# Kernel tuning notes

Measured on AMD Instinct MI355X. Metric: run time of the kernel, lower is better.

The kernel has to match this reference:

```python
import jax, jax.numpy as jnp
import numpy as np

HDIM = 1024
CDIM = 256
TEMPER = 10.0
IGNORE_OUT = 0.0
EPS = 1e-6


def setup_inputs() -> dict:
    key = jax.random.key(0)
    ks = jax.random.split(key, 6)
    B, T, D = 2, 128, 384
    x = jax.random.normal(ks[0], (B, T, D), jnp.float32)
    y = jax.random.normal(ks[1], (B, T, D), jnp.float32)
    # xavier-normal style init for the two linear layers
    W_enc = jax.random.normal(ks[2], (D, HDIM), jnp.float32) * np.sqrt(2.0 / (D + HDIM))
    b_enc = jnp.zeros((HDIM,), jnp.float32)
    W_dec = jax.random.normal(ks[3], (HDIM, D), jnp.float32) * np.sqrt(2.0 / (D + HDIM))
    b_dec = jnp.zeros((D,), jnp.float32)
    return {"x": x, "y": y, "W_enc": W_enc, "b_enc": b_enc, "W_dec": W_dec, "b_dec": b_dec}


def reference(x, y, W_enc, b_enc, W_dec, b_dec):
    B, T, D = x.shape
    n_iter = HDIM // CDIM
    pad = D - 1
    # shift_idx[s, j] = s + j : window of width D at offset s, s in [0, 2D-2]
    shift_idx = jnp.arange(2 * D - 1)[:, None] + jnp.arange(D)[None, :]

    seq_mask = (y == IGNORE_OUT)                       # (B,T,D) bool
    denom_seq = jnp.sum(~seq_mask).astype(x.dtype)
    qn = jnp.linalg.norm(y, axis=-1)                   # (B,T)

    mask_prev = None
    x_dis, losses = [], []
    for _ in range(n_iter):
        # --- _pad_for_shift: (B,T,2D-1,D) shifted windows of x ---
        kp = jnp.pad(x, ((0, 0), (0, 0), (pad, pad)))  # (B,T,3D-2)
        kpt = kp[..., shift_idx]                       # (B,T,2D-1,D)
        # --- _score (cos) + argmax over shifts ---
        kn = jnp.linalg.norm(kpt, axis=-1)             # (B,T,2D-1)
        sim = jnp.einsum('btsd,btd->bts', kpt, y) / (qn[..., None] * kn + EPS)
        sim = jnp.where(jnp.isnan(sim), 0.0, sim)
        theta = jnp.argmax(sim, axis=-1)               # (B,T) int
        x_opt = jnp.take_along_axis(kpt, theta[..., None, None], axis=-2)[..., 0, :]  # (B,T,D)
        # --- attention: elementwise cos-scaled score, temp softmax, detached ---
        dn = (jnp.linalg.norm(x_opt, axis=-1, keepdims=True)
              * jnp.linalg.norm(y, axis=-1, keepdims=True) + EPS)
        attn = jax.nn.softmax((x_opt * y / dn) / TEMPER, axis=-1)
        attn = jnp.where(jnp.isnan(attn), 0.0, attn)
        attn = jax.lax.stop_gradient(attn)
        x_attn = x_opt * attn
        # --- _reverse_pad_for_shift: window at offset 2D-2-theta ---
        kp2 = jnp.pad(x_attn, ((0, 0), (0, 0), (pad, pad)))
        rev_idx = (2 * D - 2 - theta)[..., None] + jnp.arange(D)  # (B,T,D)
        x_ele = jnp.take_along_axis(kp2, rev_idx, axis=-1)         # (B,T,D)
        # --- self_net: encoder -> top-k sparsify -> decoder_self ---
        h = x_ele @ W_enc + b_enc                      # (B,T,HDIM)
        if mask_prev is not None:
            h = jnp.where(mask_prev > 0, 1e-10, h)
        _, idx_top = jax.lax.top_k(h, CDIM)            # (B,T,CDIM)
        flat = idx_top.reshape(B * T, CDIM)
        mask_cur = jnp.zeros((B * T, HDIM), x.dtype).at[
            jnp.arange(B * T)[:, None], flat].set(1.0).reshape(B, T, HDIM)
        if mask_prev is None:
            mask_prev = mask_cur
        else:
            mask_prev = mask_prev + mask_cur - mask_prev * mask_cur
        h = h * mask_cur
        out = h @ W_dec + b_dec                        # (B,T,D)
        x_dis.append(out)
        # --- SeqLoss (masked MSE, mean-reduced by count of valid elems) ---
        err = jnp.where(seq_mask, 0.0, (out - x) ** 2) / denom_seq
        losses.append(jnp.sum(err))
    return jnp.stack(x_dis), jnp.stack(losses)
```

## Files before the change

kernel.cpp:

```cpp
#include <hip/hip_runtime.h>
#include <hip/hip_fp16.h>
#include <math.h>

#define DD 384
#define HD 1024
#define CD 256
#define NS 765
#define NITER 4
#define NROWS 256
#define TEMPER_F 10.0f
#define EPSF 1e-6f
#define CUTF 1e-10f

typedef unsigned long long u64;
typedef unsigned int u32;
typedef _Float16 hh2 __attribute__((ext_vector_type(2)));

__device__ __forceinline__ u32 flipf(float f) {
    u32 u = __float_as_uint(f);
    return u ^ ((u32)((int)u >> 31) | 0x80000000u);
}
__device__ __forceinline__ u32 packh2(float a, float b) {
    __half2 p = __floats2half2_rn(a, b);
    return __builtin_bit_cast(u32, p);
}
__device__ __forceinline__ float dot2(u32 a, u32 b, float c) {
#if __has_builtin(__builtin_amdgcn_fdot2)
    return __builtin_amdgcn_fdot2(__builtin_bit_cast(hh2, a),
                                  __builtin_bit_cast(hh2, b), c, false);
#else
    __half2 ah = __builtin_bit_cast(__half2, a);
    __half2 bh = __builtin_bit_cast(__half2, b);
    return fmaf(__half2float(ah.y), __half2float(bh.y),
           fmaf(__half2float(ah.x), __half2float(bh.x), c));
#endif
}

__global__ __launch_bounds__(256) void convert_kernel(
    const float* __restrict__ We, const float* __restrict__ Wd,
    uint4* __restrict__ wencp4, uint2* __restrict__ wd16)
{
    const int t = blockIdx.x * 256 + threadIdx.x;
    if (t < 192 * 256) {
        const int j2 = t >> 8, c4 = t & 255;
        float4 a = *(const float4*)&We[(2 * j2)     * HD + 4 * c4];
        float4 b = *(const float4*)&We[(2 * j2 + 1) * HD + 4 * c4];
        wencp4[j2 * 256 + c4] = make_uint4(packh2(a.x, b.x), packh2(a.y, b.y),
                                           packh2(a.z, b.z), packh2(a.w, b.w));
    }
    for (int i = t; i < (HD * DD) / 4; i += 65536) {
        float4 v = ((const float4*)Wd)[i];
        wd16[i] = make_uint2(packh2(v.x, v.y), packh2(v.z, v.w));
    }
}

__global__ __launch_bounds__(1024) void fused_kernel(
    const float* __restrict__ x, const float* __restrict__ y,
    const u32* __restrict__ wencp, const float* __restrict__ benc,
    const u32* __restrict__ wdec16, const float* __restrict__ bdec,
    float* __restrict__ out_xdis, float* __restrict__ lossp,
    int* __restrict__ ycnt)
{
    const int row  = blockIdx.x;
    const int tid  = threadIdx.x;
    const int lane = tid & 63;
    const int wid  = tid >> 6;

    __shared__ __align__(16) float xpad[1152];
    __shared__ __align__(16) float yr[DD];
    __shared__ float xa[DD];
    __shared__ __align__(16) float xe_s[DD];
    __shared__ u32   xep[192];
    __shared__ __align__(16) float part[4][HD];
    __shared__ __align__(16) uint2 dec2[HD];
    __shared__ __align__(16) float4 dpart[8][96];
    __shared__ float wred[16];
    __shared__ int   wredi[16];
    __shared__ float wredn[16];
    __shared__ int   wbase16[16];
    __shared__ float s_sc[4];
    __shared__ int   s_theta;
    __shared__ u32   s_b[3];
    __shared__ int   sbinB[3], srankB[3], s_cc[3];
    __shared__ u32   cand[3][64];
    __shared__ int   wcls[128];
    __shared__ int   sbase[128];
    __shared__ int   cnt8[8];
    __shared__ float loss4[NITER];

    const float* xrow = x + row * DD;
    const float* yrow = y + row * DD;

    for (int i = tid; i < 1152; i += 1024)
        xpad[i] = (i >= DD - 1 && i < 2 * DD - 1) ? xrow[i - (DD - 1)] : 0.f;
    if (tid < DD) yr[tid] = yrow[tid];
    __syncthreads();

    if (tid < DD) {
        float p = yr[tid] * yr[tid];
        int   c = (yr[tid] != 0.f) ? 1 : 0;
        for (int o = 32; o; o >>= 1) {
            p += __shfl_xor(p, o, 64);
            c += __shfl_xor(c, o, 64);
        }
        if (lane == 0) { wred[wid] = p; wredi[wid] = c; }
    }
    __syncthreads();
    if (tid == 0) {
        float s = 0.f; int c = 0;
        for (int w = 0; w < 6; ++w) { s += wred[w]; c += wredi[w]; }
        s_sc[0] = sqrtf(s);
        ycnt[row] = c;
    }
    __syncthreads();
    const float qn = s_sc[0];

    float bv = -INFINITY; int bs = 0x7fffffff; float bn = 0.f;
    if (tid < 192) {
        const float4* xp4 = (const float4*)xpad;
        const float4* yp4 = (const float4*)yr;
        float4 A = xp4[tid];
        const float f0 = A.x * A.x, f1 = A.y * A.y, f2 = A.z * A.z;
        float d0 = 0.f, d1 = 0.f, d2 = 0.f, d3 = 0.f, n0 = 0.f;
#pragma unroll 4
        for (int jc = 0; jc < 96; ++jc) {
            float4 B = xp4[tid + jc + 1];
            float4 Y = yp4[jc];
            d0 += A.x * Y.x; d0 += A.y * Y.y; d0 += A.z * Y.z; d0 += A.w * Y.w;
            d1 += A.y * Y.x; d1 += A.z * Y.y; d1 += A.w * Y.z; d1 += B.x * Y.w;
            d2 += A.z * Y.x; d2 += A.w * Y.y; d2 += B.x * Y.z; d2 += B.y * Y.w;
            d3 += A.w * Y.x; d3 += B.x * Y.y; d3 += B.y * Y.z; d3 += B.z * Y.w;
            n0 += A.x * A.x; n0 += A.y * A.y; n0 += A.z * A.z; n0 += A.w * A.w;
            A = B;
        }
        const float n1 = n0 - f0 + A.x * A.x;
        const float n2 = n1 - f1 + A.y * A.y;
        const float n3 = n2 - f2 + A.z * A.z;
        const int s0 = 4 * tid;
        float sim0 = d0 / (qn * sqrtf(n0) + EPSF);
        float sim1 = d1 / (qn * sqrtf(n1) + EPSF);
        float sim2 = d2 / (qn * sqrtf(n2) + EPSF);
        float sim3 = d3 / (qn * sqrtf(n3) + EPSF);
        bv = sim0; bs = s0; bn = n0;
        if (s0 + 1 < NS && sim1 > bv) { bv = sim1; bs = s0 + 1; bn = n1; }
        if (s0 + 2 < NS && sim2 > bv) { bv = sim2; bs = s0 + 2; bn = n2; }
        if (s0 + 3 < NS && sim3 > bv) { bv = sim3; bs = s0 + 3; bn = n3; }
    }
    for (int o = 32; o; o >>= 1) {
        float v2 = __shfl_xor(bv, o, 64);
        int   i2 = __shfl_xor(bs, o, 64);
        float n2 = __shfl_xor(bn, o, 64);
        if (v2 > bv || (v2 == bv && i2 < bs)) { bv = v2; bs = i2; bn = n2; }
    }
    if (lane == 0) { wred[wid] = bv; wredi[wid] = bs; wredn[wid] = bn; }
    __syncthreads();
    if (tid == 0) {
        float v = wred[0]; int b = wredi[0]; float nn = wredn[0];
        for (int w = 1; w < 16; ++w)
            if (wred[w] > v || (wred[w] == v && wredi[w] < b)) {
                v = wred[w]; b = wredi[w]; nn = wredn[w];
            }
        s_theta = b;
        s_sc[1] = sqrtf(nn) * qn + EPSF;
    }
    __syncthreads();
    const int theta = s_theta;
    const float dn = s_sc[1];

    float xo = 0.f, ez = 0.f;
    if (tid < DD) {
        xo = xpad[theta + tid];
        ez = expf((xo * yr[tid] / dn) / TEMPER_F);
        float p = ez;
        for (int o = 32; o; o >>= 1) p += __shfl_xor(p, o, 64);
        if (lane == 0) wred[wid] = p;
    }
    __syncthreads();
    if (tid == 0) {
        float s = 0.f;
        for (int w = 0; w < 6; ++w) s += wred[w];
        s_sc[3] = s;
    }
    __syncthreads();
    if (tid < DD) xa[tid] = xo * (ez / s_sc[3]);
    __syncthreads();
    if (tid < DD) {
        int sj = tid - (theta - (DD - 1));
        xe_s[tid] = (sj >= 0 && sj < DD) ? xa[sj] : 0.f;
    }
    __syncthreads();
    if (tid < 192) xep[tid] = packh2(xe_s[2 * tid], xe_s[2 * tid + 1]);
    __syncthreads();

    {
        const int ks = tid >> 8;
        const int c4 = tid & 255;
        const uint4* wq = (const uint4*)wencp + (size_t)(ks * 48) * 256 + c4;
        const u32* xb = xep + ks * 48;
        float4 acc = make_float4(0.f, 0.f, 0.f, 0.f);
#pragma unroll 8
        for (int j2 = 0; j2 < 48; ++j2) {
            u32 xv = xb[j2];
            uint4 w = wq[(size_t)j2 * 256];
            acc.x = dot2(xv, w.x, acc.x);
            acc.y = dot2(xv, w.y, acc.y);
            acc.z = dot2(xv, w.z, acc.z);
            acc.w = dot2(xv, w.w, acc.w);
        }
        *(float4*)&part[ks][4 * c4] = acc;
    }
    if (tid < 8) cnt8[tid] = 0;
    if (tid < NITER) loss4[tid] = 0.f;
    __syncthreads();

    const float oh = part[0][tid] + part[1][tid] + part[2][tid] + part[3][tid]
                   + benc[tid];
    const u32 okey = ~flipf(oh);
    __syncthreads();

    u32* hist = (u32*)part;
    {
        hist[tid] = 0; hist[tid + 1024] = 0;
        hist[tid + 2048] = 0; hist[tid + 3072] = 0;
        if (tid < 192) cand[tid >> 6][tid & 63] = 0xFFFFFFFFu;
        if (tid < 3) s_cc[tid] = 0;
        __syncthreads();
        atomicAdd(&hist[okey >> 20], 1u);
        __syncthreads();
        const int t4 = tid << 2;
        const u32 l0 = hist[t4], l1 = hist[t4 + 1], l2 = hist[t4 + 2], l3 = hist[t4 + 3];
        const int s = (int)(l0 + l1 + l2 + l3);
        int inc = s;
        for (int o = 1; o < 64; o <<= 1) {
            int u = __shfl_up(inc, o, 64);
            if (lane >= o) inc += u;
        }
        if (lane == 63) wredi[wid] = inc;
        __syncthreads();
        if (tid == 0) {
            int acc = 0;
            for (int w = 0; w < 16; ++w) { wbase16[w] = acc; acc += wredi[w]; }
        }
        __syncthreads();
        const int c0 = wbase16[wid] + inc - s;
        const int c1 = c0 + (int)l0, c2 = c1 + (int)l1, c3 = c2 + (int)l2;
        const int c4e = c3 + (int)l3;
#pragma unroll
        for (int i = 0; i < 3; ++i) {
            const int R = 255 + (i << 8);
            if (R >= c0 && R < c1)      { sbinB[i] = t4;     srankB[i] = R - c0; }
            else if (R >= c1 && R < c2) { sbinB[i] = t4 + 1; srankB[i] = R - c1; }
            else if (R >= c2 && R < c3) { sbinB[i] = t4 + 2; srankB[i] = R - c2; }
            else if (R >= c3 && R < c4e){ sbinB[i] = t4 + 3; srankB[i] = R - c3; }
        }
        __syncthreads();
        const int myb = (int)(okey >> 20);
#pragma unroll
        for (int i = 0; i < 3; ++i) {
            if (myb == sbinB[i]) {
                int slot = atomicAdd(&s_cc[i], 1);
                if (slot < 64) cand[i][slot] = okey;
            }
        }
        __syncthreads();
        if (wid < 3) {
            u32 v = cand[wid][lane];
            for (int k2 = 2; k2 <= 64; k2 <<= 1) {
                for (int j = k2 >> 1; j > 0; j >>= 1) {
                    u32 p = __shfl_xor(v, j, 64);
                    const bool takeMin = ((lane & j) == 0) == ((lane & k2) == 0);
                    v = takeMin ? (v < p ? v : p) : (v > p ? v : p);
                }
            }
            if (lane == srankB[wid]) s_b[wid] = v;
        }
        __syncthreads();
    }
    const u32 b1 = s_b[0], b2 = s_b[1], b3 = s_b[2];

    {
        const int myk = (okey <= b1) ? 0 : (okey <= b2) ? 1 : (okey <= b3) ? 2 : 3;
        const int cls = 2 * myk + ((oh > CUTF) ? 0 : 1);
        int myprefix = 0;
        const u64 ltmask = (1ull << lane) - 1;
#pragma unroll
        for (int c = 0; c < 8; ++c) {
            u64 m = __ballot(cls == c);
            if (cls == c) myprefix = __popcll(m & ltmask);
            if (lane == 0) {
                wcls[c * 16 + wid] = (int)__popcll(m);
                atomicAdd(&cnt8[c], (int)__popcll(m));
            }
        }
        __syncthreads();
        if (tid < 128) {
            int v = wcls[tid];
            int inc = v;
            for (int o = 1; o < 64; o <<= 1) {
                int t2 = __shfl_up(inc, o, 64);
                if (lane >= o) inc += t2;
            }
            sbase[tid] = inc - v;
        }
        __syncthreads();
        if (tid >= 64 && tid < 128) sbase[tid] += sbase[63] + wcls[63];
        __syncthreads();
        const int slot = sbase[cls * 16 + wid] + myprefix;
        dec2[slot] = make_uint2(__float_as_uint(oh), (u32)tid * 192u);
    }
    __syncthreads();

    {
        const int g8 = tid >> 7;
        const int k  = g8 >> 1;
        const int hf = g8 & 1;
        const int gg = tid & 127;
        const bool active = (gg < 96);
        int n = 0;
        if (active) n = (k == 0) ? CD : cnt8[2 * k];
        int r  = hf * 128;
        int r1 = n < r + 128 ? n : r + 128;
        if (r1 < r) r1 = r;
        float4 acc = make_float4(0.f, 0.f, 0.f, 0.f);
        const u32* wd = wdec16 + 2 * gg;
        const int base = k * CD;
        for (; r + 8 <= r1; r += 8) {
#pragma unroll
            for (int q = 0; q < 8; q += 2) {
                uint4 dv = *(const uint4*)&dec2[base + r + q];
                u32 vp = packh2(__uint_as_float(dv.x), __uint_as_float(dv.z));
                uint2 w0 = *(const uint2*)(wd + dv.y);
                uint2 w1 = *(const uint2*)(wd + dv.w);
                u32 p0 = (w0.x & 0xffffu) | (w1.x << 16);
                u32 p1 = (w0.x >> 16) | (w1.x & 0xffff0000u);
                u32 p2 = (w0.y & 0xffffu) | (w1.y << 16);
                u32 p3 = (w0.y >> 16) | (w1.y & 0xffff0000u);
                acc.x = dot2(vp, p0, acc.x);
                acc.y = dot2(vp, p1, acc.y);
                acc.z = dot2(vp, p2, acc.z);
                acc.w = dot2(vp, p3, acc.w);
            }
        }
        for (; r + 2 <= r1; r += 2) {
            uint4 dv = *(const uint4*)&dec2[base + r];
            u32 vp = packh2(__uint_as_float(dv.x), __uint_as_float(dv.z));
            uint2 w0 = *(const uint2*)(wd + dv.y);
            uint2 w1 = *(const uint2*)(wd + dv.w);
            u32 p0 = (w0.x & 0xffffu) | (w1.x << 16);
            u32 p1 = (w0.x >> 16) | (w1.x & 0xffff0000u);
            u32 p2 = (w0.y & 0xffffu) | (w1.y << 16);
            u32 p3 = (w0.y >> 16) | (w1.y & 0xffff0000u);
            acc.x = dot2(vp, p0, acc.x);
            acc.y = dot2(vp, p1, acc.y);
            acc.z = dot2(vp, p2, acc.z);
            acc.w = dot2(vp, p3, acc.w);
        }
        if (r < r1) {
            uint2 dv = dec2[base + r];
            float v0 = __uint_as_float(dv.x);
            uint2 w0 = *(const uint2*)(wd + dv.y);
            u32 vlo = packh2(v0, 0.f), vhi = packh2(0.f, v0);
            acc.x = dot2(vlo, w0.x, acc.x);
            acc.y = dot2(vhi, w0.x, acc.y);
            acc.z = dot2(vlo, w0.y, acc.z);
            acc.w = dot2(vhi, w0.y, acc.w);
        }
        if (active) dpart[g8][gg] = acc;
    }
    __syncthreads();

    {
        float l = 0.f;
        if (tid < 512) {
            const int k2 = tid >> 7;
            const int q  = tid & 127;
            if (q < 96) {
                float4 a = dpart[2 * k2][q];
                float4 b = dpart[2 * k2 + 1][q];
                float4 bb = *(const float4*)&bdec[4 * q];
                float4 o4;
                o4.x = a.x + b.x + bb.x;
                o4.y = a.y + b.y + bb.y;
                o4.z = a.z + b.z + bb.z;
                o4.w = a.w + b.w + bb.w;
                *(float4*)&out_xdis[((size_t)k2 * NROWS + row) * DD + 4 * q] = o4;
                float4 xv = *(const float4*)&xrow[4 * q];
                float4 yv = *(const float4*)&yr[4 * q];
                float ee;
                ee = o4.x - xv.x; if (yv.x != 0.f) l += ee * ee;
                ee = o4.y - xv.y; if (yv.y != 0.f) l += ee * ee;
                ee = o4.z - xv.z; if (yv.z != 0.f) l += ee * ee;
                ee = o4.w - xv.w; if (yv.w != 0.f) l += ee * ee;
            }
        }
        for (int o = 32; o; o >>= 1) l += __shfl_xor(l, o, 64);
        if (tid < 512 && lane == 0) atomicAdd(&loss4[tid >> 7], l);
    }
    __syncthreads();
    if (tid < NITER) lossp[row * NITER + tid] = loss4[tid];
}

__global__ __launch_bounds__(256) void finalize2(
    const float* __restrict__ lossp, const int* __restrict__ ycnt,
    float* __restrict__ losses)
{
    const int tid = threadIdx.x, lane = tid & 63, w = tid >> 6;
    __shared__ int ctot[4];
    int c = ycnt[tid];
    for (int o = 32; o; o >>= 1) c += __shfl_xor(c, o, 64);
    if (lane == 0) ctot[w] = c;
    __syncthreads();
    const int total = ctot[0] + ctot[1] + ctot[2] + ctot[3];
    float s = lossp[lane * NITER + w] + lossp[(lane + 64) * NITER + w]
            + lossp[(lane + 128) * NITER + w] + lossp[(lane + 192) * NITER + w];
    for (int o = 32; o; o >>= 1) s += __shfl_xor(s, o, 64);
    if (lane == 0) losses[w] = s / (float)total;
}

extern "C" void kernel_launch(void* const* d_in, const int* in_sizes, int n_in,
                              void* d_out, int out_size, void* d_ws, size_t ws_size,
                              hipStream_t stream) {
    const float* x    = (const float*)d_in[0];
    const float* y    = (const float*)d_in[1];
    const float* Wenc = (const float*)d_in[2];
    const float* benc = (const float*)d_in[3];
    const float* Wdec = (const float*)d_in[4];
    const float* bdec = (const float*)d_in[5];

    float* out  = (float*)d_out;
    float* loss = out + (out_size - NITER);

    float* lossp  = (float*)d_ws;
    int*   ycnt   = (int*)(lossp + NROWS * NITER);
    u32*   wencp  = (u32*)(ycnt + NROWS);
    u32*   wdec16 = wencp + 192 * HD;

    convert_kernel<<<256, 256, 0, stream>>>(Wenc, Wdec, (uint4*)wencp,
                                            (uint2*)wdec16);
    fused_kernel<<<NROWS, 1024, 0, stream>>>(x, y, wencp, benc, wdec16, bdec,
                                             out, lossp, ycnt);
    finalize2<<<1, 256, 0, stream>>>(lossp, ycnt, loss);
}
```

Before: 100.2 us.

## Split shift-score dot products across 768 threads and cut barriers in prologue

The 384-long cross-correlation per shift is now split into four quarter chunks handled by 768 threads, with partial sums combined through a new shared buffer. The y-norm reduction and the zeroing of the histogram and scratch state run on the otherwise idle threads during the same phase. The softmax normalisation and reverse shift are folded into a single packing step, and the histogram gets its own shared buffer so it no longer needs a separate clear-and-barrier phase. Together these remove several __syncthreads and serial tid==0 steps, in exchange for more shared memory (which may lower occupancy) and some recomputed expf calls.

```diff
diff --git a/kernel.cpp b/kernel.cpp
--- a/kernel.cpp
+++ b/kernel.cpp
@@ -68,10 +68,10 @@
 
     __shared__ __align__(16) float xpad[1152];
     __shared__ __align__(16) float yr[DD];
-    __shared__ float xa[DD];
-    __shared__ __align__(16) float xe_s[DD];
     __shared__ u32   xep[192];
     __shared__ __align__(16) float part[4][HD];
+    __shared__ __align__(16) u32   hist2[4096];
+    __shared__ float spart[4 * 192 * 5];
     __shared__ __align__(16) uint2 dec2[HD];
     __shared__ __align__(16) float4 dpart[8][96];
     __shared__ float wred[16];
@@ -96,36 +96,17 @@
     if (tid < DD) yr[tid] = yrow[tid];
     __syncthreads();
 
-    if (tid < DD) {
-        float p = yr[tid] * yr[tid];
-        int   c = (yr[tid] != 0.f) ? 1 : 0;
-        for (int o = 32; o; o >>= 1) {
-            p += __shfl_xor(p, o, 64);
-            c += __shfl_xor(c, o, 64);
-        }
-        if (lane == 0) { wred[wid] = p; wredi[wid] = c; }
-    }
-    __syncthreads();
-    if (tid == 0) {
-        float s = 0.f; int c = 0;
-        for (int w = 0; w < 6; ++w) { s += wred[w]; c += wredi[w]; }
-        s_sc[0] = sqrtf(s);
-        ycnt[row] = c;
-    }
-    __syncthreads();
-    const float qn = s_sc[0];
-
-    float bv = -INFINITY; int bs = 0x7fffffff; float bn = 0.f;
-    if (tid < 192) {
+    if (tid < 768) {
+        const int qid = tid / 192, t = tid - qid * 192;
+        const int jb = 24 * qid;
         const float4* xp4 = (const float4*)xpad;
         const float4* yp4 = (const float4*)yr;
-        float4 A = xp4[tid];
-        const float f0 = A.x * A.x, f1 = A.y * A.y, f2 = A.z * A.z;
+        float4 A = xp4[t + jb];
         float d0 = 0.f, d1 = 0.f, d2 = 0.f, d3 = 0.f, n0 = 0.f;
-#pragma unroll 4
-        for (int jc = 0; jc < 96; ++jc) {
-            float4 B = xp4[tid + jc + 1];
-            float4 Y = yp4[jc];
+#pragma unroll 8
+        for (int jc = 0; jc < 24; ++jc) {
+            float4 B = xp4[t + jb + jc + 1];
+            float4 Y = yp4[jb + jc];
             d0 += A.x * Y.x; d0 += A.y * Y.y; d0 += A.z * Y.z; d0 += A.w * Y.w;
             d1 += A.y * Y.x; d1 += A.z * Y.y; d1 += A.w * Y.z; d1 += B.x * Y.w;
             d2 += A.z * Y.x; d2 += A.w * Y.y; d2 += B.x * Y.z; d2 += B.y * Y.w;
@@ -133,63 +114,101 @@
             n0 += A.x * A.x; n0 += A.y * A.y; n0 += A.z * A.z; n0 += A.w * A.w;
             A = B;
         }
-        const float n1 = n0 - f0 + A.x * A.x;
-        const float n2 = n1 - f1 + A.y * A.y;
-        const float n3 = n2 - f2 + A.z * A.z;
+        float* sp = &spart[(qid * 192 + t) * 5];
+        sp[0] = d0; sp[1] = d1; sp[2] = d2; sp[3] = d3; sp[4] = n0;
+    } else {
+        const int i = tid - 768;
+        if (i < 192) {
+            float y0 = yr[2 * i], y1 = yr[2 * i + 1];
+            float p = y0 * y0 + y1 * y1;
+            int   c = (y0 != 0.f) + (y1 != 0.f);
+            for (int o = 32; o; o >>= 1) {
+                p += __shfl_xor(p, o, 64);
+                c += __shfl_xor(c, o, 64);
+            }
+            if (lane == 0) { wred[wid] = p; wredi[wid] = c; }
+            cand[i >> 6][i & 63] = 0xFFFFFFFFu;
+        } else {
+            const int j = i - 192;
+            if (j < 3) s_cc[j] = 0;
+            else if (j < 11) cnt8[j - 3] = 0;
+            else if (j < 15) loss4[j - 11] = 0.f;
+        }
+        for (int h = i; h < 4096; h += 256) hist2[h] = 0u;
+    }
+    __syncthreads();
+
+    if (tid < 192) {
+        const float qn = sqrtf(wred[12] + wred[13] + wred[14]);
+        const int b = tid * 5;
+        float d0 = spart[b]     + spart[b + 960]     + spart[b + 1920]     + spart[b + 2880];
+        float d1 = spart[b + 1] + spart[b + 961]     + spart[b + 1921]     + spart[b + 2881];
+        float d2 = spart[b + 2] + spart[b + 962]     + spart[b + 1922]     + spart[b + 2882];
+        float d3 = spart[b + 3] + spart[b + 963]     + spart[b + 1923]     + spart[b + 2883];
+        float n0 = spart[b + 4] + spart[b + 964]     + spart[b + 1924]     + spart[b + 2884];
+        const float x0 = xpad[4 * tid],       x1 = xpad[4 * tid + 1], x2 = xpad[4 * tid + 2];
+        const float e0 = xpad[4 * tid + 384], e1 = xpad[4 * tid + 385], e2 = xpad[4 * tid + 386];
+        const float n1 = n0 - x0 * x0 + e0 * e0;
+        const float n2 = n1 - x1 * x1 + e1 * e1;
+        const float n3 = n2 - x2 * x2 + e2 * e2;
         const int s0 = 4 * tid;
         float sim0 = d0 / (qn * sqrtf(n0) + EPSF);
         float sim1 = d1 / (qn * sqrtf(n1) + EPSF);
         float sim2 = d2 / (qn * sqrtf(n2) + EPSF);
         float sim3 = d3 / (qn * sqrtf(n3) + EPSF);
-        bv = sim0; bs = s0; bn = n0;
+        float bv = sim0; int bs = s0; float bn = n0;
         if (s0 + 1 < NS && sim1 > bv) { bv = sim1; bs = s0 + 1; bn = n1; }
         if (s0 + 2 < NS && sim2 > bv) { bv = sim2; bs = s0 + 2; bn = n2; }
         if (s0 + 3 < NS && sim3 > bv) { bv = sim3; bs = s0 + 3; bn = n3; }
-    }
-    for (int o = 32; o; o >>= 1) {
-        float v2 = __shfl_xor(bv, o, 64);
-        int   i2 = __shfl_xor(bs, o, 64);
-        float n2 = __shfl_xor(bn, o, 64);
-        if (v2 > bv || (v2 == bv && i2 < bs)) { bv = v2; bs = i2; bn = n2; }
-    }
-    if (lane == 0) { wred[wid] = bv; wredi[wid] = bs; wredn[wid] = bn; }
-    __syncthreads();
+        for (int o = 32; o; o >>= 1) {
+            float v2 = __shfl_xor(bv, o, 64);
+            int   i2 = __shfl_xor(bs, o, 64);
+            float nn2 = __shfl_xor(bn, o, 64);
+            if (v2 > bv || (v2 == bv && i2 < bs)) { bv = v2; bs = i2; bn = nn2; }
+        }
+        if (lane == 0) { wred[wid] = bv; wredi[wid] = bs; wredn[wid] = bn; }
+        if (tid == 0) s_sc[0] = qn;
+    }
+    if (tid == 960) ycnt[row] = wredi[12] + wredi[13] + wredi[14];
+    __syncthreads();
+
     if (tid == 0) {
         float v = wred[0]; int b = wredi[0]; float nn = wredn[0];
-        for (int w = 1; w < 16; ++w)
+        for (int w = 1; w < 3; ++w)
             if (wred[w] > v || (wred[w] == v && wredi[w] < b)) {
                 v = wred[w]; b = wredi[w]; nn = wredn[w];
             }
         s_theta = b;
-        s_sc[1] = sqrtf(nn) * qn + EPSF;
+        s_sc[1] = sqrtf(nn) * s_sc[0] + EPSF;
     }
     __syncthreads();
     const int theta = s_theta;
     const float dn = s_sc[1];
 
-    float xo = 0.f, ez = 0.f;
     if (tid < DD) {
-        xo = xpad[theta + tid];
-        ez = expf((xo * yr[tid] / dn) / TEMPER_F);
+        float xo = xpad[theta + tid];
+        float ez = expf((xo * yr[tid] / dn) / TEMPER_F);
         float p = ez;
         for (int o = 32; o; o >>= 1) p += __shfl_xor(p, o, 64);
         if (lane == 0) wred[wid] = p;
     }
     __syncthreads();
-    if (tid == 0) {
-        float s = 0.f;
-        for (int w = 0; w < 6; ++w) s += wred[w];
-        s_sc[3] = s;
-    }
-    __syncthreads();
-    if (tid < DD) xa[tid] = xo * (ez / s_sc[3]);
-    __syncthreads();
-    if (tid < DD) {
-        int sj = tid - (theta - (DD - 1));
-        xe_s[tid] = (sj >= 0 && sj < DD) ? xa[sj] : 0.f;
-    }
-    __syncthreads();
-    if (tid < 192) xep[tid] = packh2(xe_s[2 * tid], xe_s[2 * tid + 1]);
+
+    if (tid < 192) {
+        const float S = wred[0] + wred[1] + wred[2] + wred[3] + wred[4] + wred[5];
+        const int off = theta - (DD - 1);
+        const int sj = 2 * tid - off;
+        float a0 = 0.f, a1 = 0.f;
+        if (sj >= 0 && sj < DD) {
+            float xo = xpad[theta + sj];
+            a0 = xo * (expf((xo * yr[sj] / dn) / TEMPER_F) / S);
+        }
+        if (sj + 1 >= 0 && sj + 1 < DD) {
+            float xo = xpad[theta + sj + 1];
+            a1 = xo * (expf((xo * yr[sj + 1] / dn) / TEMPER_F) / S);
+        }
+        xep[tid] = packh2(a0, a1);
+    }
     __syncthreads();
 
     {
@@ -209,26 +228,17 @@
         }
         *(float4*)&part[ks][4 * c4] = acc;
     }
-    if (tid < 8) cnt8[tid] = 0;
-    if (tid < NITER) loss4[tid] = 0.f;
     __syncthreads();
 
     const float oh = part[0][tid] + part[1][tid] + part[2][tid] + part[3][tid]
                    + benc[tid];
     const u32 okey = ~flipf(oh);
-    __syncthreads();
-
-    u32* hist = (u32*)part;
+    atomicAdd(&hist2[okey >> 20], 1u);
+    __syncthreads();
+
     {
-        hist[tid] = 0; hist[tid + 1024] = 0;
-        hist[tid + 2048] = 0; hist[tid + 3072] = 0;
-        if (tid < 192) cand[tid >> 6][tid & 63] = 0xFFFFFFFFu;
-        if (tid < 3) s_cc[tid] = 0;
-        __syncthreads();
-        atomicAdd(&hist[okey >> 20], 1u);
-        __syncthreads();
         const int t4 = tid << 2;
-        const u32 l0 = hist[t4], l1 = hist[t4 + 1], l2 = hist[t4 + 2], l3 = hist[t4 + 3];
+        const u32 l0 = hist2[t4], l1 = hist2[t4 + 1], l2 = hist2[t4 + 2], l3 = hist2[t4 + 3];
         const int s = (int)(l0 + l1 + l2 + l3);
         int inc = s;
         for (int o = 1; o < 64; o <<= 1) {
```

Result: no change. 99.24 us (-0.9%).
